# Kernel optimization log

Hardware: AMD Instinct MI355X
Metric: run time of the kernel (lower is better)

## Reference

```python
import jax, jax.numpy as jnp
import numpy as np

N_NODES = 50000
N_EDGES = 800000
IN_DIM = 128
HID = 64
OUT_DIM = 128
N_GRAPHS = 256


def setup_inputs() -> dict:
    key = jax.random.key(0)
    ks = jax.random.split(key, 8)
    x = jax.random.normal(ks[0], (N_NODES, IN_DIM), dtype=jnp.float32)
    edge_index = jax.random.randint(ks[1], (2, N_EDGES), 0, N_NODES, dtype=jnp.int64)
    batch = jnp.sort(jax.random.randint(ks[2], (N_NODES,), 0, N_GRAPHS, dtype=jnp.int64))
    # Glorot-ish init for GCN weights, zero bias (PyG default bias=True)
    W1 = jax.random.normal(ks[3], (IN_DIM, HID), dtype=jnp.float32) / np.sqrt(IN_DIM)
    b1 = jnp.zeros((HID,), dtype=jnp.float32)
    W2 = jax.random.normal(ks[4], (HID, HID), dtype=jnp.float32) / np.sqrt(HID)
    b2 = jnp.zeros((HID,), dtype=jnp.float32)
    W3 = jax.random.normal(ks[5], (HID, OUT_DIM), dtype=jnp.float32) / np.sqrt(HID)
    b3 = jnp.zeros((OUT_DIM,), dtype=jnp.float32)
    return {"x": x, "edge_index": edge_index, "batch": batch, "num_graphs": N_GRAPHS,
            "W1": W1, "b1": b1, "W2": W2, "b2": b2, "W3": W3, "b3": b3}


def _gcn_norm(edge_index, n_nodes):
    # PyG GCNConv default: add self-loops, symmetric D^{-1/2}(A+I)D^{-1/2} norm.
    loops = jnp.arange(n_nodes, dtype=edge_index.dtype)
    src = jnp.concatenate([edge_index[0], loops])  # [E + N]
    dst = jnp.concatenate([edge_index[1], loops])
    deg = jax.ops.segment_sum(jnp.ones_like(dst, dtype=jnp.float32), dst,
                              num_segments=n_nodes)
    dinv = jnp.where(deg > 0, jax.lax.rsqrt(jnp.maximum(deg, 1.0)), 0.0)
    norm = dinv[src] * dinv[dst]  # [E + N]
    return src, dst, norm


def _gcn_conv(x, W, b, src, dst, norm, n_nodes):
    h = x @ W                                  # [N, F_out] dense GEMM
    msg = h[src] * norm[:, None]               # gather + scale  [E+N, F_out]
    agg = jax.ops.segment_sum(msg, dst, num_segments=n_nodes)
    return agg + b


def reference(x, edge_index, batch, num_graphs, W1, b1, W2, b2, W3, b3):
    n_nodes = x.shape[0]
    src, dst, norm = _gcn_norm(edge_index, n_nodes)
    h = jax.nn.gelu(_gcn_conv(x, W1, b1, src, dst, norm, n_nodes))
    h = jax.nn.gelu(_gcn_conv(h, W2, b2, src, dst, norm, n_nodes))
    h = _gcn_conv(h, W3, b3, src, dst, norm, n_nodes)
    # global_mean_pool over batch segment ids
    sums = jax.ops.segment_sum(h, batch, num_segments=num_graphs)
    counts = jax.ops.segment_sum(jnp.ones((n_nodes,), dtype=h.dtype), batch,
                                 num_segments=num_graphs)
    return sums / jnp.maximum(counts, 1.0)[:, None]
```

## Files before the change

kernel.cpp:

```cpp
#include <hip/hip_runtime.h>
#include <hip/hip_fp16.h>
#include <math.h>

#define N_NODES   50000
#define N_EDGES   800000
#define IN_DIM    128
#define HID       64
#define OUT_DIM   128
#define N_GRAPHS  256
#define MAX_DEG   64
#define PARTS     8
#define PSIZE     (N_NODES / PARTS)
#define EPB       4096
#define AGG_NPB   32
#define DEGP      32

typedef _Float16 half8 __attribute__((ext_vector_type(8)));
typedef float floatx4 __attribute__((ext_vector_type(4)));


__global__ __launch_bounds__(256) void k_build(const int* __restrict__ src,
                                               const int* __restrict__ dst,
                                               int* __restrict__ deg, int* __restrict__ col) {
    int p     = blockIdx.x & (PARTS - 1);
    int chunk = blockIdx.x >> 3;
    int e0    = chunk * EPB + threadIdx.x * 16;
    if (e0 + 16 > N_EDGES) return;
    int lo = p * PSIZE, hi = lo + PSIZE;

    int dd[16], ss[16];
    const int4* d4 = (const int4*)(dst + e0);
    const int4* s4 = (const int4*)(src + e0);
#pragma unroll
    for (int j = 0; j < 4; j++) {
        int4 q = d4[j];
        dd[4 * j + 0] = q.x; dd[4 * j + 1] = q.y;
        dd[4 * j + 2] = q.z; dd[4 * j + 3] = q.w;
    }
#pragma unroll
    for (int j = 0; j < 4; j++) {
        int4 q = s4[j];
        ss[4 * j + 0] = q.x; ss[4 * j + 1] = q.y;
        ss[4 * j + 2] = q.z; ss[4 * j + 3] = q.w;
    }

    int pos[16];
#pragma unroll
    for (int j = 0; j < 16; j++) {
        pos[j] = -1;
        if (dd[j] >= lo && dd[j] < hi) pos[j] = atomicAdd(&deg[(size_t)dd[j] * DEGP], 1);
    }
#pragma unroll
    for (int j = 0; j < 16; j++) {
        if (pos[j] >= 0 && pos[j] < MAX_DEG)
            col[(size_t)dd[j] * MAX_DEG + pos[j]] = ss[j];
    }
}

__global__ __launch_bounds__(256) void k_prep(const int* __restrict__ deg,
                                              int* __restrict__ degc,
                                              float* __restrict__ dinv,
                                              const float* __restrict__ W1, __half* __restrict__ Wt1,
                                              const float* __restrict__ W2, __half* __restrict__ Wt2) {
    int blk = blockIdx.x;
    if (blk < 196) {
        int n = blk * 256 + threadIdx.x;
        if (n < N_NODES) {
            int dg = deg[(size_t)n * DEGP];
            degc[n] = dg;
            dinv[n] = rsqrtf((float)(dg + 1));
        }
    } else if (blk < 200) {
        int idx = (blk - 196) * 256 + threadIdx.x;
        int g = idx >> 6, n = idx & 63;
#pragma unroll
        for (int i = 0; i < 8; i++)
            Wt1[idx * 8 + i] = __float2half(W1[(8 * g + i) * 64 + n]);
    } else {
        int idx = (blk - 200) * 256 + threadIdx.x;
        if (idx < 512) {
            int g = idx >> 6, n = idx & 63;
#pragma unroll
            for (int i = 0; i < 8; i++)
                Wt2[idx * 8 + i] = __float2half(W2[(8 * g + i) * 64 + n]);
        }
    }
}


__global__ __launch_bounds__(256) void k_mfma1(const float* __restrict__ A,
                                               const float* __restrict__ dinv,
                                               const __half* __restrict__ Bp,
                                               __half* __restrict__ C) {
    constexpr int K = IN_DIM, S = K / 32;
    int wv   = threadIdx.x >> 6;
    int lane = threadIdx.x & 63;
    int quad = lane >> 4, l15 = lane & 15;
    int row0 = blockIdx.x * 64 + wv * 16;
    if (row0 >= N_NODES) return;

    half8 bf[S][4];
#pragma unroll
    for (int s = 0; s < S; s++)
#pragma unroll
        for (int j = 0; j < 4; j++)
            bf[s][j] = *(const half8*)(Bp + ((size_t)((4 * s + quad) * 64 + 16 * j + l15)) * 8);

    floatx4 acc[4];
#pragma unroll
    for (int j = 0; j < 4; j++) acc[j] = 0.f;

    int arow = row0 + l15;
    float dv = dinv[arow];
#pragma unroll
    for (int s = 0; s < S; s++) {
        float4 xa = *(const float4*)(A + (size_t)arow * K + 32 * s + quad * 8);
        float4 xb = *(const float4*)(A + (size_t)arow * K + 32 * s + quad * 8 + 4);
        half8 af;
        af[0] = (_Float16)(xa.x * dv); af[1] = (_Float16)(xa.y * dv);
        af[2] = (_Float16)(xa.z * dv); af[3] = (_Float16)(xa.w * dv);
        af[4] = (_Float16)(xb.x * dv); af[5] = (_Float16)(xb.y * dv);
        af[6] = (_Float16)(xb.z * dv); af[7] = (_Float16)(xb.w * dv);
#pragma unroll
        for (int j = 0; j < 4; j++)
            acc[j] = __builtin_amdgcn_mfma_f32_16x16x32_f16(af, bf[s][j], acc[j], 0, 0, 0);
    }
#pragma unroll
    for (int j = 0; j < 4; j++)
#pragma unroll
        for (int r = 0; r < 4; r++)
            C[(size_t)(row0 + quad * 4 + r) * 64 + 16 * j + l15] = __float2half(acc[j][r]);
}


__global__ __launch_bounds__(256) void k_mfma2(const __half* __restrict__ A,
                                               const __half* __restrict__ Bp,
                                               __half* __restrict__ C) {
    constexpr int K = HID, S = K / 32;
    int wv   = threadIdx.x >> 6;
    int lane = threadIdx.x & 63;
    int quad = lane >> 4, l15 = lane & 15;
    int row0 = blockIdx.x * 64 + wv * 16;
    if (row0 >= N_NODES) return;

    half8 bf[S][4];
#pragma unroll
    for (int s = 0; s < S; s++)
#pragma unroll
        for (int j = 0; j < 4; j++)
            bf[s][j] = *(const half8*)(Bp + ((size_t)((4 * s + quad) * 64 + 16 * j + l15)) * 8);

    floatx4 acc[4];
#pragma unroll
    for (int j = 0; j < 4; j++) acc[j] = 0.f;

    int arow = row0 + l15;
#pragma unroll
    for (int s = 0; s < S; s++) {
        half8 af = *(const half8*)(A + (size_t)arow * K + 32 * s + quad * 8);
#pragma unroll
        for (int j = 0; j < 4; j++)
            acc[j] = __builtin_amdgcn_mfma_f32_16x16x32_f16(af, bf[s][j], acc[j], 0, 0, 0);
    }
#pragma unroll
    for (int j = 0; j < 4; j++)
#pragma unroll
        for (int r = 0; r < 4; r++)
            C[(size_t)(row0 + quad * 4 + r) * 64 + 16 * j + l15] = __float2half(acc[j][r]);
}


__device__ __forceinline__ void add8(float* acc, uint4 v) {
    const __half2* h = (const __half2*)&v;
#pragma unroll
    for (int j = 0; j < 4; j++) {
        acc[2 * j]     += __low2float(h[j]);
        acc[2 * j + 1] += __high2float(h[j]);
    }
}

__global__ __launch_bounds__(256) void k_agg(const __half* __restrict__ T,
                                             const int* __restrict__ col,
                                             const int* __restrict__ indeg,
                                             const float* __restrict__ dinv,
                                             const float* __restrict__ b,
                                             __half* __restrict__ OUT, int mode) {
    __shared__ int cols[AGG_NPB][MAX_DEG + 1];
    __shared__ int sdeg[AGG_NPB];
    int base = blockIdx.x * AGG_NPB;

    if (threadIdx.x < AGG_NPB) {
        int g = base + threadIdx.x;
        int dg0 = (g < N_NODES) ? indeg[g] : 0;
        sdeg[threadIdx.x] = dg0 > MAX_DEG ? MAX_DEG : dg0;
    }
    __syncthreads();

    for (int idx = threadIdx.x; idx < AGG_NPB * MAX_DEG; idx += 256) {
        int r = idx >> 6, j = idx & 63;
        if (j < sdeg[r]) cols[r][j] = col[(size_t)(base + r) * MAX_DEG + j];
    }
    __syncthreads();

    int lane = threadIdx.x & 63;
    int wv   = threadIdx.x >> 6;
    int q = lane >> 3, t = lane & 7;
    int local = wv * 8 + q;
    int d = base + local;
    if (d >= N_NODES) return;

    int dg = sdeg[local];

    float acc[8];
#pragma unroll
    for (int j = 0; j < 8; j++) acc[j] = 0.f;
    add8(acc, *(const uint4*)(T + (size_t)d * HID + t * 8));

    const int* cl = cols[local];
    int i = 0;
    for (; i + 4 <= dg; i += 4) {
        int s0 = cl[i], s1 = cl[i + 1], s2 = cl[i + 2], s3 = cl[i + 3];
        uint4 v0 = *(const uint4*)(T + (size_t)s0 * HID + t * 8);
        uint4 v1 = *(const uint4*)(T + (size_t)s1 * HID + t * 8);
        uint4 v2 = *(const uint4*)(T + (size_t)s2 * HID + t * 8);
        uint4 v3 = *(const uint4*)(T + (size_t)s3 * HID + t * 8);
        add8(acc, v0); add8(acc, v1); add8(acc, v2); add8(acc, v3);
    }
    for (; i < dg; i++) {
        int s = cl[i];
        add8(acc, *(const uint4*)(T + (size_t)s * HID + t * 8));
    }

    float dv = dinv[d];
    float o[8];
#pragma unroll
    for (int j = 0; j < 8; j++) o[j] = acc[j] * dv;
    if (mode == 0) {
#pragma unroll
        for (int j = 0; j < 8; j++) {
            float v = o[j] + b[t * 8 + j];
            float u2 = 0.7978845608028654f * (v + 0.044715f * v * v * v);
            float th = 1.0f - 2.0f / (__expf(2.0f * u2) + 1.0f);
            o[j] = 0.5f * v * (1.0f + th) * dv;
        }
    }
    __half2 hh[4];
#pragma unroll
    for (int j = 0; j < 4; j++) hh[j] = __floats2half2_rn(o[2 * j], o[2 * j + 1]);
    *(uint4*)(OUT + (size_t)d * HID + t * 8) = *(uint4*)hh;
}


__global__ __launch_bounds__(256) void k_pool_out(const __half* __restrict__ A,
                                                  const int* __restrict__ batch,
                                                  const float* __restrict__ W3,
                                                  const float* __restrict__ b3,
                                                  float* __restrict__ out) {
    int g = blockIdx.x;
    int lo = 0, hi = N_NODES;
    while (lo < hi) { int m = (lo + hi) >> 1; if (batch[m] < g) lo = m + 1; else hi = m; }
    int lo2 = lo, hi2 = N_NODES;
    while (lo2 < hi2) { int m = (lo2 + hi2) >> 1; if (batch[m] < g + 1) lo2 = m + 1; else hi2 = m; }
    int start = lo, end = lo2;

    int lane = threadIdx.x & 63;
    int wave = threadIdx.x >> 6;
    float acc = 0.f;
    for (int n = start + wave; n < end; n += 4)
        acc += __half2float(A[(size_t)n * HID + lane]);

    __shared__ float part[4][HID];
    __shared__ float pooled[HID];
    part[wave][lane] = acc;
    __syncthreads();
    if (threadIdx.x < HID)
        pooled[threadIdx.x] = part[0][threadIdx.x] + part[1][threadIdx.x] +
                              part[2][threadIdx.x] + part[3][threadIdx.x];
    __syncthreads();

    if (threadIdx.x < OUT_DIM) {
        float cntf = (float)(end - start);
        float inv = 1.0f / fmaxf(cntf, 1.0f);
        float s = 0.f;
#pragma unroll
        for (int k = 0; k < HID; k++) s += pooled[k] * W3[k * OUT_DIM + threadIdx.x];
        out[g * OUT_DIM + threadIdx.x] = (s + cntf * b3[threadIdx.x]) * inv;
    }
}


extern "C" void kernel_launch(void* const* d_in, const int* in_sizes, int n_in,
                              void* d_out, int out_size, void* d_ws, size_t ws_size,
                              hipStream_t stream) {
    const float* x     = (const float*)d_in[0];
    const int*   ei    = (const int*)d_in[1];
    const int*   batch = (const int*)d_in[2];
    const float* W1    = (const float*)d_in[4];
    const float* b1    = (const float*)d_in[5];
    const float* W2    = (const float*)d_in[6];
    const float* b2    = (const float*)d_in[7];
    const float* W3    = (const float*)d_in[8];
    const float* b3    = (const float*)d_in[9];
    float* out = (float*)d_out;

    const int* esrc = ei;
    const int* edst = ei + N_EDGES;

    int*    deg  = (int*)d_ws;
    int*    degc = deg + (size_t)N_NODES * DEGP;
    float*  dinv = (float*)(degc + N_NODES);
    int*    col  = (int*)(dinv + N_NODES);
    __half* t    = (__half*)(col + (size_t)N_NODES * MAX_DEG);
    __half* p    = t + (size_t)N_NODES * HID;
    __half* Wt1  = p + (size_t)N_NODES * HID;
    __half* Wt2  = Wt1 + IN_DIM * HID;

    (void)hipMemsetAsync(deg, 0, (size_t)N_NODES * DEGP * 4, stream);

    const int CHUNKS = (N_EDGES + EPB - 1) / EPB;
    k_build<<<CHUNKS * PARTS, 256, 0, stream>>>(esrc, edst, deg, col);
    k_prep<<<202, 256, 0, stream>>>(deg, degc, dinv, W1, Wt1, W2, Wt2);

    const int GB = (N_NODES + 63) / 64;
    const int AB = (N_NODES + AGG_NPB - 1) / AGG_NPB;

    k_mfma1<<<GB, 256, 0, stream>>>(x, dinv, Wt1, t);
    k_agg<<<AB, 256, 0, stream>>>(t, col, degc, dinv, b1, p, 0);
    k_mfma2<<<GB, 256, 0, stream>>>(p, Wt2, t);
    k_agg<<<AB, 256, 0, stream>>>(t, col, degc, dinv, b2, p, 0);
    k_agg<<<AB, 256, 0, stream>>>(p, col, degc, dinv, b3, t, 1);
    k_pool_out<<<N_GRAPHS, 256, 0, stream>>>(t, batch, W3, b3, out);
}
```

Before: 215.8 us.

## Overlap first GEMM with CSR build and apply degree scaling afterward

Merges the layer-1 GEMM and the edge-bucketing build into one launch so they run concurrently. To make this possible, the D^{-1/2} scaling moves out of the GEMM input into a separate pass that rescales the fp16 GEMM output once degrees are known. W1 is converted to fp16 and laid out in LDS per block instead of by a prep kernel. The cost is an extra read-modify-write over the N×64 fp16 intermediate, a slightly different rounding order, and repeated per-block W1 conversion.

Result: no change. 214.8 us (-0.4%).

```diff
diff --git a/kernel.cpp b/kernel.cpp
--- a/kernel.cpp
+++ b/kernel.cpp
@@ -14,70 +14,148 @@
 #define EPB       4096
 #define AGG_NPB   32
 #define DEGP      32
+#define GEMM_BLKS 782
 
 typedef _Float16 half8 __attribute__((ext_vector_type(8)));
 typedef float floatx4 __attribute__((ext_vector_type(4)));
 
 
-__global__ __launch_bounds__(256) void k_build(const int* __restrict__ src,
-                                               const int* __restrict__ dst,
-                                               int* __restrict__ deg, int* __restrict__ col) {
-    int p     = blockIdx.x & (PARTS - 1);
-    int chunk = blockIdx.x >> 3;
-    int e0    = chunk * EPB + threadIdx.x * 16;
-    if (e0 + 16 > N_EDGES) return;
-    int lo = p * PSIZE, hi = lo + PSIZE;
-
-    int dd[16], ss[16];
-    const int4* d4 = (const int4*)(dst + e0);
-    const int4* s4 = (const int4*)(src + e0);
-#pragma unroll
-    for (int j = 0; j < 4; j++) {
-        int4 q = d4[j];
-        dd[4 * j + 0] = q.x; dd[4 * j + 1] = q.y;
-        dd[4 * j + 2] = q.z; dd[4 * j + 3] = q.w;
-    }
-#pragma unroll
-    for (int j = 0; j < 4; j++) {
-        int4 q = s4[j];
-        ss[4 * j + 0] = q.x; ss[4 * j + 1] = q.y;
-        ss[4 * j + 2] = q.z; ss[4 * j + 3] = q.w;
-    }
-
-    int pos[16];
-#pragma unroll
-    for (int j = 0; j < 16; j++) {
-        pos[j] = -1;
-        if (dd[j] >= lo && dd[j] < hi) pos[j] = atomicAdd(&deg[(size_t)dd[j] * DEGP], 1);
-    }
-#pragma unroll
-    for (int j = 0; j < 16; j++) {
-        if (pos[j] >= 0 && pos[j] < MAX_DEG)
-            col[(size_t)dd[j] * MAX_DEG + pos[j]] = ss[j];
-    }
-}
-
-__global__ __launch_bounds__(256) void k_prep(const int* __restrict__ deg,
-                                              int* __restrict__ degc,
-                                              float* __restrict__ dinv,
-                                              const float* __restrict__ W1, __half* __restrict__ Wt1,
-                                              const float* __restrict__ W2, __half* __restrict__ Wt2) {
+__global__ __launch_bounds__(256) void k_fused1(const float* __restrict__ A,
+                                                const float* __restrict__ W1,
+                                                __half* __restrict__ C,
+                                                const int* __restrict__ src,
+                                                const int* __restrict__ dst,
+                                                int* __restrict__ deg,
+                                                int* __restrict__ col) {
+    if (blockIdx.x < GEMM_BLKS) {
+        constexpr int K = IN_DIM, S = K / 32;
+        __shared__ __half wlds[IN_DIM * HID];
+
+#pragma unroll
+        for (int u = 0; u < 8; u++) {
+            int o = threadIdx.x * 32 + u * 4;
+            float4 w = *(const float4*)(W1 + o);
+            int k = o >> 6, n = o & 63;
+            int bi = (((k >> 3) * 64) + n) * 8 + (k & 7);
+            wlds[bi]      = __float2half(w.x);
+            wlds[bi + 8]  = __float2half(w.y);
+            wlds[bi + 16] = __float2half(w.z);
+            wlds[bi + 24] = __float2half(w.w);
+        }
+        __syncthreads();
+
+        int wv   = threadIdx.x >> 6;
+        int lane = threadIdx.x & 63;
+        int quad = lane >> 4, l15 = lane & 15;
+        int row0 = blockIdx.x * 64 + wv * 16;
+        if (row0 >= N_NODES) return;
+
+        half8 bf[S][4];
+#pragma unroll
+        for (int s = 0; s < S; s++)
+#pragma unroll
+            for (int j = 0; j < 4; j++)
+                bf[s][j] = *(const half8*)&wlds[(((4 * s + quad) * 64) + 16 * j + l15) * 8];
+
+        floatx4 acc[4];
+#pragma unroll
+        for (int j = 0; j < 4; j++) acc[j] = 0.f;
+
+        int arow = row0 + l15;
+#pragma unroll
+        for (int s = 0; s < S; s++) {
+            float4 xa = *(const float4*)(A + (size_t)arow * K + 32 * s + quad * 8);
+            float4 xb = *(const float4*)(A + (size_t)arow * K + 32 * s + quad * 8 + 4);
+            half8 af;
+            af[0] = (_Float16)xa.x; af[1] = (_Float16)xa.y;
+            af[2] = (_Float16)xa.z; af[3] = (_Float16)xa.w;
+            af[4] = (_Float16)xb.x; af[5] = (_Float16)xb.y;
+            af[6] = (_Float16)xb.z; af[7] = (_Float16)xb.w;
+#pragma unroll
+            for (int j = 0; j < 4; j++)
+                acc[j] = __builtin_amdgcn_mfma_f32_16x16x32_f16(af, bf[s][j], acc[j], 0, 0, 0);
+        }
+#pragma unroll
+        for (int j = 0; j < 4; j++)
+#pragma unroll
+            for (int r = 0; r < 4; r++)
+                C[(size_t)(row0 + quad * 4 + r) * 64 + 16 * j + l15] = __float2half(acc[j][r]);
+    } else {
+        int bid   = blockIdx.x - GEMM_BLKS;
+        int p     = bid & (PARTS - 1);
+        int chunk = bid >> 3;
+        int e0    = chunk * EPB + threadIdx.x * 16;
+        if (e0 + 16 > N_EDGES) return;
+        int lo = p * PSIZE, hi = lo + PSIZE;
+
+        int dd[16], ss[16];
+        const int4* d4 = (const int4*)(dst + e0);
+        const int4* s4 = (const int4*)(src + e0);
+#pragma unroll
+        for (int j = 0; j < 4; j++) {
+            int4 q = d4[j];
+            dd[4 * j + 0] = q.x; dd[4 * j + 1] = q.y;
+            dd[4 * j + 2] = q.z; dd[4 * j + 3] = q.w;
+        }
+#pragma unroll
+        for (int j = 0; j < 4; j++) {
+            int4 q = s4[j];
+            ss[4 * j + 0] = q.x; ss[4 * j + 1] = q.y;
+            ss[4 * j + 2] = q.z; ss[4 * j + 3] = q.w;
+        }
+
+        int pos[16];
+#pragma unroll
+        for (int j = 0; j < 16; j++) {
+            pos[j] = -1;
+            if (dd[j] >= lo && dd[j] < hi) pos[j] = atomicAdd(&deg[(size_t)dd[j] * DEGP], 1);
+        }
+#pragma unroll
+        for (int j = 0; j < 16; j++) {
+            if (pos[j] >= 0 && pos[j] < MAX_DEG)
+                col[(size_t)dd[j] * MAX_DEG + pos[j]] = ss[j];
+        }
+    }
+}
+
+
+__global__ __launch_bounds__(256) void k_scale(const int* __restrict__ deg,
+                                               int* __restrict__ degc,
+                                               float* __restrict__ dinv,
+                                               __half* __restrict__ t,
+                                               const float* __restrict__ W2,
+                                               __half* __restrict__ Wt2) {
     int blk = blockIdx.x;
     if (blk < 196) {
-        int n = blk * 256 + threadIdx.x;
+        __shared__ float sdv[256];
+        int n0 = blk * 256;
+        int n = n0 + threadIdx.x;
+        float dv = 1.f;
         if (n < N_NODES) {
             int dg = deg[(size_t)n * DEGP];
             degc[n] = dg;
-            dinv[n] = rsqrtf((float)(dg + 1));
-        }
-    } else if (blk < 200) {
+            dv = rsqrtf((float)(dg + 1));
+            dinv[n] = dv;
+        }
+        sdv[threadIdx.x] = dv;
+        __syncthreads();
+#pragma unroll
+        for (int it = 0; it < 8; it++) {
+            int idx = it * 256 + threadIdx.x;
+            int r = idx >> 3, c = idx & 7;
+            int node = n0 + r;
+            if (node < N_NODES) {
+                uint4 v = *(const uint4*)(t + (size_t)node * HID + c * 8);
+                float w = sdv[r];
+                __half2* h = (__half2*)&v;
+#pragma unroll
+                for (int j = 0; j < 4; j++)
+                    h[j] = __floats2half2_rn(__low2float(h[j]) * w, __high2float(h[j]) * w);
+                *(uint4*)(t + (size_t)node * HID + c * 8) = v;
+            }
+        }
+    } else {
         int idx = (blk - 196) * 256 + threadIdx.x;
-        int g = idx >> 6, n = idx & 63;
-#pragma unroll
-        for (int i = 0; i < 8; i++)
-            Wt1[idx * 8 + i] = __float2half(W1[(8 * g + i) * 64 + n]);
-    } else {
-        int idx = (blk - 200) * 256 + threadIdx.x;
         if (idx < 512) {
             int g = idx >> 6, n = idx & 63;
 #pragma unroll
@@ -85,51 +163,6 @@
                 Wt2[idx * 8 + i] = __float2half(W2[(8 * g + i) * 64 + n]);
         }
     }
-}
-
-
-__global__ __launch_bounds__(256) void k_mfma1(const float* __restrict__ A,
-                                               const float* __restrict__ dinv,
-                                               const __half* __restrict__ Bp,
-                                               __half* __restrict__ C) {
-    constexpr int K = IN_DIM, S = K / 32;
-    int wv   = threadIdx.x >> 6;
-    int lane = threadIdx.x & 63;
-    int quad = lane >> 4, l15 = lane & 15;
-    int row0 = blockIdx.x * 64 + wv * 16;
-    if (row0 >= N_NODES) return;
-
-    half8 bf[S][4];
-#pragma unroll
-    for (int s = 0; s < S; s++)
-#pragma unroll
-        for (int j = 0; j < 4; j++)
-            bf[s][j] = *(const half8*)(Bp + ((size_t)((4 * s + quad) * 64 + 16 * j + l15)) * 8);
-
-    floatx4 acc[4];
-#pragma unroll
-    for (int j = 0; j < 4; j++) acc[j] = 0.f;
-
-    int arow = row0 + l15;
-    float dv = dinv[arow];
-#pragma unroll
-    for (int s = 0; s < S; s++) {
-        float4 xa = *(const float4*)(A + (size_t)arow * K + 32 * s + quad * 8);
-        float4 xb = *(const float4*)(A + (size_t)arow * K + 32 * s + quad * 8 + 4);
-        half8 af;
-        af[0] = (_Float16)(xa.x * dv); af[1] = (_Float16)(xa.y * dv);
-        af[2] = (_Float16)(xa.z * dv); af[3] = (_Float16)(xa.w * dv);
-        af[4] = (_Float16)(xb.x * dv); af[5] = (_Float16)(xb.y * dv);
-        af[6] = (_Float16)(xb.z * dv); af[7] = (_Float16)(xb.w * dv);
-#pragma unroll
-        for (int j = 0; j < 4; j++)
-            acc[j] = __builtin_amdgcn_mfma_f32_16x16x32_f16(af, bf[s][j], acc[j], 0, 0, 0);
-    }
-#pragma unroll
-    for (int j = 0; j < 4; j++)
-#pragma unroll
-        for (int r = 0; r < 4; r++)
-            C[(size_t)(row0 + quad * 4 + r) * 64 + 16 * j + l15] = __float2half(acc[j][r]);
 }
 
 
@@ -312,21 +345,18 @@
     int*    col  = (int*)(dinv + N_NODES);
     __half* t    = (__half*)(col + (size_t)N_NODES * MAX_DEG);
     __half* p    = t + (size_t)N_NODES * HID;
-    __half* Wt1  = p + (size_t)N_NODES * HID;
-    __half* Wt2  = Wt1 + IN_DIM * HID;
+    __half* Wt2  = p + (size_t)N_NODES * HID;
 
     (void)hipMemsetAsync(deg, 0, (size_t)N_NODES * DEGP * 4, stream);
 
     const int CHUNKS = (N_EDGES + EPB - 1) / EPB;
-    k_build<<<CHUNKS * PARTS, 256, 0, stream>>>(esrc, edst, deg, col);
-    k_prep<<<202, 256, 0, stream>>>(deg, degc, dinv, W1, Wt1, W2, Wt2);
-
-    const int GB = (N_NODES + 63) / 64;
     const int AB = (N_NODES + AGG_NPB - 1) / AGG_NPB;
 
-    k_mfma1<<<GB, 256, 0, stream>>>(x, dinv, Wt1, t);
+    k_fused1<<<GEMM_BLKS + CHUNKS * PARTS, 256, 0, stream>>>(x, W1, t, esrc, edst, deg, col);
+    k_scale<<<198, 256, 0, stream>>>(deg, degc, dinv, t, W2, Wt2);
+
     k_agg<<<AB, 256, 0, stream>>>(t, col, degc, dinv, b1, p, 0);
-    k_mfma2<<<GB, 256, 0, stream>>>(p, Wt2, t);
+    k_mfma2<<<GEMM_BLKS, 256, 0, stream>>>(p, Wt2, t);
     k_agg<<<AB, 256, 0, stream>>>(t, col, degc, dinv, b2, p, 0);
     k_agg<<<AB, 256, 0, stream>>>(p, col, degc, dinv, b3, t, 1);
     k_pool_out<<<N_GRAPHS, 256, 0, stream>>>(t, batch, W3, b3, out);
```
